# Performance work log

Measured on AMD Instinct MI355X. Metric: run time of the kernel, lower is better.

Reference implementation:

```python
import jax, jax.numpy as jnp
import numpy as np

B = 4_194_304  # batch size


def setup_inputs() -> dict:
    key = jax.random.key(0)
    k1, k2, k3, k4 = jax.random.split(key, 4)
    X = jax.random.normal(k1, (B, 4), dtype=jnp.float32)
    mu = jax.random.normal(k2, (B, 2), dtype=jnp.float32)
    sigma = jax.random.uniform(k3, (B,), dtype=jnp.float32)
    u = jax.random.normal(k4, (B, 2), dtype=jnp.float32)
    Q = jnp.array([[1.0, 0.0, 0.0, 0.0],
                   [0.0, 1.0, 0.0, 0.0],
                   [0.0, 0.0, 0.5, 0.0],
                   [0.0, 0.0, 0.0, 0.5]], dtype=jnp.float32)
    R = jnp.array([[0.1, 0.0], [0.0, 0.1]], dtype=jnp.float32)
    x_target = jnp.array([1.0, 0.0, 0.0, 0.0], dtype=jnp.float32)
    return {"X": X, "mu": mu, "sigma": sigma, "u": u,
            "Q": Q, "R": R, "x_target": x_target}


def reference(X, mu, sigma, u, Q, R, x_target):
    omega = 0.6
    # Hard-coded system matrices from HJBModel.__init__
    f = jnp.array([[0.0, 0.0, 1.0, 0.0],
                   [0.0, 0.0, 0.0, 1.0],
                   [0.0, omega, 0.0, 0.0],
                   [-omega, 0.0, 0.0, 0.0]], dtype=X.dtype)
    G = jnp.array([[0.3, 0.0], [0.0, 0.25], [1.0, 0.0], [0.0, 1.0]], dtype=X.dtype)
    COV = jnp.array([[0.0, 0.0], [0.0, 0.0], [0.5, 0.0], [0.0, 0.5]], dtype=X.dtype)

    xr = X - x_target                                    # [B,4]
    # V = xr^T Q xr
    V = jnp.einsum('bi,ij,bj->b', xr, Q, xr)             # [B]
    # dyn = f X + G u + COV mu
    dyn = X @ f.T + u @ G.T + mu @ COV.T                 # [B,4]
    # grad1 @ dyn = 2 xr^T Q dyn
    g1dyn = 2.0 * jnp.einsum('bi,ij,bj->b', xr, Q, dyn)  # [B]
    # 0.5 u^T R u
    uRu = 0.5 * jnp.einsum('bi,ij,bj->b', u, R, u)       # [B]
    # trace term: 0.5 sigma^2 * trace(2Q @ COV COV^T)
    tr_const = jnp.trace((2.0 * Q) @ (COV @ COV.T))      # scalar
    trace_term = 0.5 * sigma ** 2 * tr_const             # [B]
    return jnp.mean(g1dyn + V + uRu + trace_term)
```

## Files before the change

kernel.cpp:

```cpp
#include <hip/hip_runtime.h>

#define BLOCK 256
#define GRID  8192

typedef float vf4 __attribute__((ext_vector_type(4)));
typedef float vf2 __attribute__((ext_vector_type(2)));

__device__ __forceinline__ float uniform_f(float v) {
    return __int_as_float(__builtin_amdgcn_readfirstlane(__float_as_int(v)));
}

__device__ __forceinline__ float row_val(
    float x0, float x1, float x2, float x3,
    float u0, float u1, float m0, float m1, float sg,
    const float* q, float r0, float r1, float r2, float r3,
    float t0, float t1, float t2, float t3, float tr_c)
{
    float xr0 = x0 - t0, xr1 = x1 - t1, xr2 = x2 - t2, xr3 = x3 - t3;
    float dyn0 = x2 + 0.3f * u0;
    float dyn1 = x3 + 0.25f * u1;
    float dyn2 = 0.6f * x1 + u0 + 0.5f * m0;
    float dyn3 = -0.6f * x0 + u1 + 0.5f * m1;
    float qx0 = xr0 * q[0] + xr1 * q[4] + xr2 * q[8]  + xr3 * q[12];
    float qx1 = xr0 * q[1] + xr1 * q[5] + xr2 * q[9]  + xr3 * q[13];
    float qx2 = xr0 * q[2] + xr1 * q[6] + xr2 * q[10] + xr3 * q[14];
    float qx3 = xr0 * q[3] + xr1 * q[7] + xr2 * q[11] + xr3 * q[15];
    float V    = qx0 * xr0 + qx1 * xr1 + qx2 * xr2 + qx3 * xr3;
    float g1   = 2.0f * (qx0 * dyn0 + qx1 * dyn1 + qx2 * dyn2 + qx3 * dyn3);
    float uRu  = 0.5f * (u0 * (r0 * u0 + r1 * u1) + u1 * (r2 * u0 + r3 * u1));
    float tt   = 0.5f * sg * sg * tr_c;
    return V + g1 + uRu + tt;
}

__global__ __launch_bounds__(BLOCK, 8) void hjb_loss_kernel(
    const float* __restrict__ X,
    const float* __restrict__ mu,
    const float* __restrict__ sigma,
    const float* __restrict__ u,
    const float* __restrict__ Q,
    const float* __restrict__ R,
    const float* __restrict__ xt,
    float* __restrict__ partials,
    int npairs, float inv_B)
{
    float q[16];
#pragma unroll
    for (int i = 0; i < 16; ++i) q[i] = uniform_f(Q[i]);
    const float r0 = uniform_f(R[0]), r1 = uniform_f(R[1]);
    const float r2 = uniform_f(R[2]), r3 = uniform_f(R[3]);
    const float t0 = uniform_f(xt[0]), t1 = uniform_f(xt[1]);
    const float t2 = uniform_f(xt[2]), t3 = uniform_f(xt[3]);
    const float tr_c = 0.5f * (q[10] + q[15]);

    const vf4* __restrict__ X4  = reinterpret_cast<const vf4*>(X);
    const vf4* __restrict__ u4  = reinterpret_cast<const vf4*>(u);
    const vf4* __restrict__ mu4 = reinterpret_cast<const vf4*>(mu);
    const vf2* __restrict__ s2  = reinterpret_cast<const vf2*>(sigma);

    float acc = 0.0f;
    const int tid = blockIdx.x * BLOCK + threadIdx.x;
    const int T   = gridDim.x * BLOCK;

    for (int p = tid; p < npairs; p += T) {
        vf4 xa = __builtin_nontemporal_load(&X4[2 * p + 0]);
        vf4 xb = __builtin_nontemporal_load(&X4[2 * p + 1]);
        vf4 uu = __builtin_nontemporal_load(&u4[p]);
        vf4 mm = __builtin_nontemporal_load(&mu4[p]);
        vf2 ss = __builtin_nontemporal_load(&s2[p]);

        acc += row_val(xa.x, xa.y, xa.z, xa.w, uu.x, uu.y, mm.x, mm.y, ss.x,
                       q, r0, r1, r2, r3, t0, t1, t2, t3, tr_c);
        acc += row_val(xb.x, xb.y, xb.z, xb.w, uu.z, uu.w, mm.z, mm.w, ss.y,
                       q, r0, r1, r2, r3, t0, t1, t2, t3, tr_c);
    }

    acc *= inv_B;

#pragma unroll
    for (int off = 32; off > 0; off >>= 1)
        acc += __shfl_down(acc, off, 64);

    __shared__ float wave_sums[BLOCK / 64];
    const int lane = threadIdx.x & 63;
    const int wid  = threadIdx.x >> 6;
    if (lane == 0) wave_sums[wid] = acc;
    __syncthreads();

    if (wid == 0) {
        float v = (lane < BLOCK / 64) ? wave_sums[lane] : 0.0f;
        v += __shfl_down(v, 2, 64);
        v += __shfl_down(v, 1, 64);
        if (lane == 0) partials[blockIdx.x] = v;
    }
}

__global__ __launch_bounds__(BLOCK) void hjb_finish_kernel(
    const float* __restrict__ partials, float* __restrict__ out, int n)
{
    float acc = 0.0f;
    for (int i = threadIdx.x; i < n; i += BLOCK)
        acc += partials[i];
#pragma unroll
    for (int off = 32; off > 0; off >>= 1)
        acc += __shfl_down(acc, off, 64);

    __shared__ float wave_sums[BLOCK / 64];
    const int lane = threadIdx.x & 63;
    const int wid  = threadIdx.x >> 6;
    if (lane == 0) wave_sums[wid] = acc;
    __syncthreads();

    if (wid == 0) {
        float v = (lane < BLOCK / 64) ? wave_sums[lane] : 0.0f;
        v += __shfl_down(v, 2, 64);
        v += __shfl_down(v, 1, 64);
        if (lane == 0) out[0] = v;
    }
}

extern "C" void kernel_launch(void* const* d_in, const int* in_sizes, int n_in,
                              void* d_out, int out_size, void* d_ws, size_t ws_size,
                              hipStream_t stream) {
    const float* X     = (const float*)d_in[0];
    const float* mu    = (const float*)d_in[1];
    const float* sigma = (const float*)d_in[2];
    const float* u     = (const float*)d_in[3];
    const float* Q     = (const float*)d_in[4];
    const float* R     = (const float*)d_in[5];
    const float* xt    = (const float*)d_in[6];
    float* out = (float*)d_out;
    float* partials = (float*)d_ws;

    const int B = in_sizes[2];
    const int npairs = B / 2;
    const float inv_B = 1.0f / (float)B;

    hjb_loss_kernel<<<GRID, BLOCK, 0, stream>>>(
        X, mu, sigma, u, Q, R, xt, partials, npairs, inv_B);
    hjb_finish_kernel<<<1, BLOCK, 0, stream>>>(partials, out, GRID);
}
```

Measured before the change: 164.9 us.

## Software-pipeline loads in grid-stride loop with smaller grid

Measured after the change: 158.5 us. -3.9%, faster.

```diff
diff --git a/kernel.cpp b/kernel.cpp
--- a/kernel.cpp
+++ b/kernel.cpp
@@ -1,13 +1,39 @@
 #include <hip/hip_runtime.h>
 
 #define BLOCK 256
-#define GRID  8192
+#define GRID  1024
 
 typedef float vf4 __attribute__((ext_vector_type(4)));
 typedef float vf2 __attribute__((ext_vector_type(2)));
 
 __device__ __forceinline__ float uniform_f(float v) {
     return __int_as_float(__builtin_amdgcn_readfirstlane(__float_as_int(v)));
+}
+
+struct Chunk {
+    vf4 xa0, xa1, xb0, xb1;
+    vf4 uua, uub;
+    vf4 mma, mmb;
+    vf2 ssa, ssb;
+};
+
+__device__ __forceinline__ Chunk load_chunk(
+    const vf4* __restrict__ X4, const vf4* __restrict__ u4,
+    const vf4* __restrict__ mu4, const vf2* __restrict__ s2,
+    int pa, int pb)
+{
+    Chunk c;
+    c.xa0 = __builtin_nontemporal_load(&X4[2 * pa + 0]);
+    c.xa1 = __builtin_nontemporal_load(&X4[2 * pa + 1]);
+    c.xb0 = __builtin_nontemporal_load(&X4[2 * pb + 0]);
+    c.xb1 = __builtin_nontemporal_load(&X4[2 * pb + 1]);
+    c.uua = __builtin_nontemporal_load(&u4[pa]);
+    c.uub = __builtin_nontemporal_load(&u4[pb]);
+    c.mma = __builtin_nontemporal_load(&mu4[pa]);
+    c.mmb = __builtin_nontemporal_load(&mu4[pb]);
+    c.ssa = __builtin_nontemporal_load(&s2[pa]);
+    c.ssb = __builtin_nontemporal_load(&s2[pb]);
+    return c;
 }
 
 __device__ __forceinline__ float row_val(
@@ -32,7 +58,24 @@
     return V + g1 + uRu + tt;
 }
 
-__global__ __launch_bounds__(BLOCK, 8) void hjb_loss_kernel(
+__device__ __forceinline__ float chunk_val(
+    const Chunk& c, const float* q,
+    float r0, float r1, float r2, float r3,
+    float t0, float t1, float t2, float t3, float tr_c)
+{
+    float a = 0.0f;
+    a += row_val(c.xa0.x, c.xa0.y, c.xa0.z, c.xa0.w, c.uua.x, c.uua.y,
+                 c.mma.x, c.mma.y, c.ssa.x, q, r0, r1, r2, r3, t0, t1, t2, t3, tr_c);
+    a += row_val(c.xa1.x, c.xa1.y, c.xa1.z, c.xa1.w, c.uua.z, c.uua.w,
+                 c.mma.z, c.mma.w, c.ssa.y, q, r0, r1, r2, r3, t0, t1, t2, t3, tr_c);
+    a += row_val(c.xb0.x, c.xb0.y, c.xb0.z, c.xb0.w, c.uub.x, c.uub.y,
+                 c.mmb.x, c.mmb.y, c.ssb.x, q, r0, r1, r2, r3, t0, t1, t2, t3, tr_c);
+    a += row_val(c.xb1.x, c.xb1.y, c.xb1.z, c.xb1.w, c.uub.z, c.uub.w,
+                 c.mmb.z, c.mmb.w, c.ssb.y, q, r0, r1, r2, r3, t0, t1, t2, t3, tr_c);
+    return a;
+}
+
+__global__ __launch_bounds__(BLOCK, 4) void hjb_loss_kernel(
     const float* __restrict__ X,
     const float* __restrict__ mu,
     const float* __restrict__ sigma,
@@ -61,13 +104,24 @@
     const int tid = blockIdx.x * BLOCK + threadIdx.x;
     const int T   = gridDim.x * BLOCK;
 
-    for (int p = tid; p < npairs; p += T) {
+    int p = tid;
+    if (p + T < npairs) {
+        Chunk cur = load_chunk(X4, u4, mu4, s2, p, p + T);
+        p += 2 * T;
+        while (p + T < npairs) {
+            Chunk nxt = load_chunk(X4, u4, mu4, s2, p, p + T);
+            acc += chunk_val(cur, q, r0, r1, r2, r3, t0, t1, t2, t3, tr_c);
+            cur = nxt;
+            p += 2 * T;
+        }
+        acc += chunk_val(cur, q, r0, r1, r2, r3, t0, t1, t2, t3, tr_c);
+    }
+    for (; p < npairs; p += T) {
         vf4 xa = __builtin_nontemporal_load(&X4[2 * p + 0]);
         vf4 xb = __builtin_nontemporal_load(&X4[2 * p + 1]);
         vf4 uu = __builtin_nontemporal_load(&u4[p]);
         vf4 mm = __builtin_nontemporal_load(&mu4[p]);
         vf2 ss = __builtin_nontemporal_load(&s2[p]);
-
         acc += row_val(xa.x, xa.y, xa.z, xa.w, uu.x, uu.y, mm.x, mm.y, ss.x,
                        q, r0, r1, r2, r3, t0, t1, t2, t3, tr_c);
         acc += row_val(xb.x, xb.y, xb.z, xb.w, uu.z, uu.w, mm.z, mm.w, ss.y,
```
